# Optimization experiments

Hardware: AMD Instinct MI355X
Metric: run time of the kernel (lower is better)

Reference implementation:

```python
import jax, jax.numpy as jnp
import numpy as np

R = 4          # self.radius
NS = 256       # self.out_num_samples


def conv2d(x, w, b=None, padding=1, dilation=1):
    out = jax.lax.conv_general_dilated(
        x, w, window_strides=(1, 1),
        padding=[(padding, padding), (padding, padding)],
        rhs_dilation=(dilation, dilation),
        dimension_numbers=('NCHW', 'OIHW', 'NCHW'))
    if b is not None:
        out = out + b[None, :, None, None]
    return out


def depth_regression(logits):
    # softmax over 256 depth hypotheses, then expectation over a 9-wide
    # window centered at the argmax (clamped to [0, NS-1]).
    prob = jax.nn.softmax(logits, axis=1)                      # [B,256,H,W]
    amax = jnp.argmax(prob, axis=1, keepdims=True)             # [B,1,H,W] int
    offs = jnp.arange(-R, R + 1).reshape(1, 2 * R + 1, 1, 1)
    idx = jnp.clip(amax + offs, 0, NS - 1)                     # [B,9,H,W]
    p = jnp.take_along_axis(prob, idx, axis=1)                 # [B,9,H,W]
    num = jnp.sum(idx.astype(prob.dtype) * p, axis=1, keepdims=True)
    den = 1e-6 + jnp.sum(p, axis=1, keepdims=True)
    nd = (num / den) / (NS - 1.0)                              # [B,1,H,W]
    return nd, prob


def setup_inputs() -> dict:
    key = jax.random.key(0)
    ks = jax.random.split(key, 16)
    B, H, W = 4, 256, 320
    HD = 32            # hidden_dim
    CD = 32            # corr channels; input_dim = CD + 1 = 33
    CIN = HD + 1 + CD  # 65, GRU conv input channels

    def w(k, shape):
        fan = int(np.prod(shape[1:]))
        return (jax.random.normal(k, shape, jnp.float32) / np.sqrt(fan)).astype(jnp.float32)

    return {
        'hidden': jnp.tanh(jax.random.normal(ks[0], (B, HD, H, W), jnp.float32)),
        'normalized_depth': jax.random.uniform(ks[1], (B, 1, H, W), dtype=jnp.float32),
        'corr': jax.random.normal(ks[2], (B, CD, H, W), jnp.float32),
        # ConvGRU params (3x3, padding 1, with bias)
        'convz_w': w(ks[3], (HD, CIN, 3, 3)), 'convz_b': jnp.zeros((HD,), jnp.float32),
        'convr_w': w(ks[4], (HD, CIN, 3, 3)), 'convr_b': jnp.zeros((HD,), jnp.float32),
        'convq_w': w(ks[5], (HD, CIN, 3, 3)), 'convq_b': jnp.zeros((HD,), jnp.float32),
        # depth_head: 3x3 dil2 (no bias) -> 1x1 (no bias) -> 1x1 (bias)
        'dh1_w': w(ks[6], (32, HD, 3, 3)),
        'dh2_w': w(ks[7], (64, 32, 1, 1)),
        'dh3_w': w(ks[8], (NS, 64, 1, 1)), 'dh3_b': jnp.zeros((NS,), jnp.float32),
        # confidence_head: 3x3 dil2 (no bias) -> 1x1 (bias)
        'ch1_w': w(ks[9], (32, HD, 3, 3)),
        'ch2_w': w(ks[10], (1, 32, 1, 1)), 'ch2_b': jnp.zeros((1,), jnp.float32),
    }


def reference(hidden, normalized_depth, corr,
              convz_w, convz_b, convr_w, convr_b, convq_w, convq_b,
              dh1_w, dh2_w, dh3_w, dh3_b, ch1_w, ch2_w, ch2_b):
    # cat = [normalized_depth, corr]
    x = jnp.concatenate([normalized_depth, corr], axis=1)      # [B,33,H,W]
    # ConvGRU (confidence=None branch)
    hx = jnp.concatenate([hidden, x], axis=1)                  # [B,65,H,W]
    z = jax.nn.sigmoid(conv2d(hx, convz_w, convz_b))
    r = jax.nn.sigmoid(conv2d(hx, convr_w, convr_b))
    q = jnp.tanh(conv2d(jnp.concatenate([r * hidden, x], axis=1), convq_w, convq_b))
    h = (1.0 - z) * hidden + z * q                             # [B,32,H,W]
    # confidence head (confidence_flag=True)
    conf0 = conv2d(jax.nn.relu(conv2d(h, ch1_w, padding=2, dilation=2)),
                   ch2_w, ch2_b, padding=0)                    # [B,1,H,W]
    conf = jax.nn.sigmoid(conf0)
    # depth head
    t = jax.nn.relu(conv2d(h, dh1_w, padding=2, dilation=2))
    t = jax.nn.relu(conv2d(t, dh2_w, padding=0))
    logits = conv2d(t, dh3_w, dh3_b, padding=0)                # [B,256,H,W]
    nd, prob = depth_regression(logits)
    return h, nd, prob, conf, conf0
```

## Files before the change

### kernel.cpp

```cpp
#include <hip/hip_runtime.h>

#define WDT 320
#define HGT 256
#define HWSZ 81920
#define NPIX 327680

__device__ __forceinline__ float sigm(float x){ return 1.0f/(1.0f + __expf(-x)); }
__device__ __forceinline__ float tanh_(float x){
  float e = __expf(-2.0f*fabsf(x));
  float t = (1.0f - e)/(1.0f + e);
  return x < 0.0f ? -t : t;
}

__global__ __launch_bounds__(256) void k_wprep(
    const float* __restrict__ zw, const float* __restrict__ rw,
    const float* __restrict__ qw, const float* __restrict__ d1w,
    const float* __restrict__ c1w, const float* __restrict__ d2w,
    const float* __restrict__ d3w,
    float* __restrict__ W1, float* __restrict__ W2, float* __restrict__ W3,
    float* __restrict__ Wd2, float* __restrict__ Wd3)
{
  const int N1 = 9*65*64, N2 = 9*65*32, N3 = 9*32*64, N4 = 32*64, N5 = 64*256;
  int i = blockIdx.x*256 + threadIdx.x;
  if (i < N1){
    int cin = i / 576, r = i % 576;
    int tap = r >> 6, co = r & 63;
    float v = (co < 32) ? zw[(size_t)(co*65 + cin)*9 + tap]
                        : rw[(size_t)((co-32)*65 + cin)*9 + tap];
    W1[i] = v;
  } else if (i < N1 + N2){
    int j = i - N1;
    int cin = j / 288, r = j % 288;
    int tap = r >> 5, co = r & 31;
    W2[j] = qw[(size_t)(co*65 + cin)*9 + tap];
  } else if (i < N1 + N2 + N3){
    int j = i - (N1 + N2);
    int cin = j / 576, r = j % 576;
    int tap = r >> 6, co = r & 63;
    float v = (co < 32) ? d1w[(size_t)(co*32 + cin)*9 + tap]
                        : c1w[(size_t)((co-32)*32 + cin)*9 + tap];
    W3[j] = v;
  } else if (i < N1 + N2 + N3 + N4){
    int j = i - (N1 + N2 + N3);
    int cin = j >> 6, co = j & 63;
    Wd2[j] = d2w[co*32 + cin];
  } else if (i < N1 + N2 + N3 + N4 + N5){
    int j = i - (N1 + N2 + N3 + N4);
    int cin = j >> 8, co = j & 255;
    Wd3[j] = d3w[co*64 + cin];
  }
}


__global__ __launch_bounds__(256) void k_gru1(
    const float* __restrict__ hidden, const float* __restrict__ ndp,
    const float* __restrict__ corr, const float* __restrict__ W1,
    const float* __restrict__ zb, const float* __restrict__ rb,
    float* __restrict__ zpl, float* __restrict__ rhpl)
{
  int bid = blockIdx.x;
  int pb = (bid & 7)*160 + (bid >> 3);
  int p = pb*256 + threadIdx.x;
  int row = p / WDT;
  int x = p - row*WDT;
  int yimg = row & (HGT-1);
  int b = __builtin_amdgcn_readfirstlane(row >> 8);
  int q = p - b*HWSZ;
  int vo[9]; float mf[9];
  #pragma unroll
  for (int ty=0; ty<3; ++ty){
    #pragma unroll
    for (int tx=0; tx<3; ++tx){
      int dy = ty-1, dx = tx-1;
      bool ok = ((unsigned)(yimg+dy) < (unsigned)HGT) && ((unsigned)(x+dx) < (unsigned)WDT);
      vo[ty*3+tx] = ok ? (q + dy*WDT + dx) : q;
      mf[ty*3+tx] = ok ? 1.0f : 0.0f;
    }
  }
  const float* hb = hidden + (size_t)b*32*HWSZ;
  const float* cb = corr   + (size_t)b*32*HWSZ;
  const float* nb = ndp    + (size_t)b*HWSZ;
  float acc[64];
  #pragma unroll
  for (int i=0;i<64;++i) acc[i]=0.f;
  #pragma unroll 1
  for (int c=0;c<32;++c){
    const float* src = hb + (size_t)c*HWSZ;
    const float* wr  = W1 + c*576;
    #pragma unroll
    for (int t=0;t<9;++t){
      float vv = src[vo[t]] * mf[t];
      const float* w = wr + t*64;
      #pragma unroll
      for (int i=0;i<64;++i) acc[i] = fmaf(w[i], vv, acc[i]);
    }
  }
  {
    const float* wr = W1 + 32*576;
    #pragma unroll
    for (int t=0;t<9;++t){
      float vv = nb[vo[t]] * mf[t];
      const float* w = wr + t*64;
      #pragma unroll
      for (int i=0;i<64;++i) acc[i] = fmaf(w[i], vv, acc[i]);
    }
  }
  #pragma unroll 1
  for (int c=0;c<32;++c){
    const float* src = cb + (size_t)c*HWSZ;
    const float* wr  = W1 + (33+c)*576;
    #pragma unroll
    for (int t=0;t<9;++t){
      float vv = src[vo[t]] * mf[t];
      const float* w = wr + t*64;
      #pragma unroll
      for (int i=0;i<64;++i) acc[i] = fmaf(w[i], vv, acc[i]);
    }
  }
  #pragma unroll
  for (int c=0;c<32;++c)
    zpl[(size_t)c*NPIX + p] = sigm(acc[c] + zb[c]);
  #pragma unroll
  for (int c=0;c<32;++c){
    float r = sigm(acc[32+c] + rb[c]);
    rhpl[(size_t)c*NPIX + p] = r * hb[q + (size_t)c*HWSZ];
  }
}

__global__ __launch_bounds__(256) void k_gru2(
    const float* __restrict__ hidden, const float* __restrict__ ndp,
    const float* __restrict__ corr, const float* __restrict__ rhpl,
    const float* __restrict__ zpl, const float* __restrict__ W2,
    const float* __restrict__ qb, float* __restrict__ out_h)
{
  int bid = blockIdx.x;
  int pb = (bid & 7)*160 + (bid >> 3);
  int p = pb*256 + threadIdx.x;
  int row = p / WDT;
  int x = p - row*WDT;
  int yimg = row & (HGT-1);
  int b = __builtin_amdgcn_readfirstlane(row >> 8);
  int q = p - b*HWSZ;
  int vo[9]; float mf[9];
  #pragma unroll
  for (int ty=0; ty<3; ++ty){
    #pragma unroll
    for (int tx=0; tx<3; ++tx){
      int dy = ty-1, dx = tx-1;
      bool ok = ((unsigned)(yimg+dy) < (unsigned)HGT) && ((unsigned)(x+dx) < (unsigned)WDT);
      vo[ty*3+tx] = ok ? (q + dy*WDT + dx) : q;
      mf[ty*3+tx] = ok ? 1.0f : 0.0f;
    }
  }
  const float* hb = hidden + (size_t)b*32*HWSZ;
  const float* cb = corr   + (size_t)b*32*HWSZ;
  const float* nb = ndp    + (size_t)b*HWSZ;
  const float* rb_ = rhpl  + (size_t)b*HWSZ;
  float acc[32];
  #pragma unroll
  for (int i=0;i<32;++i) acc[i]=0.f;
  #pragma unroll 1
  for (int c=0;c<32;++c){
    const float* src = rb_ + (size_t)c*NPIX;
    const float* wr  = W2 + c*288;
    #pragma unroll
    for (int t=0;t<9;++t){
      float vv = src[vo[t]] * mf[t];
      const float* w = wr + t*32;
      #pragma unroll
      for (int i=0;i<32;++i) acc[i] = fmaf(w[i], vv, acc[i]);
    }
  }
  {
    const float* wr = W2 + 32*288;
    #pragma unroll
    for (int t=0;t<9;++t){
      float vv = nb[vo[t]] * mf[t];
      const float* w = wr + t*32;
      #pragma unroll
      for (int i=0;i<32;++i) acc[i] = fmaf(w[i], vv, acc[i]);
    }
  }
  #pragma unroll 1
  for (int c=0;c<32;++c){
    const float* src = cb + (size_t)c*HWSZ;
    const float* wr  = W2 + (33+c)*288;
    #pragma unroll
    for (int t=0;t<9;++t){
      float vv = src[vo[t]] * mf[t];
      const float* w = wr + t*32;
      #pragma unroll
      for (int i=0;i<32;++i) acc[i] = fmaf(w[i], vv, acc[i]);
    }
  }
  #pragma unroll
  for (int c=0;c<32;++c){
    float qv = tanh_(acc[c] + qb[c]);
    float z  = zpl[(size_t)c*NPIX + p];
    float h0 = hb[q + (size_t)c*HWSZ];
    out_h[(size_t)b*32*HWSZ + (size_t)c*HWSZ + q] = (1.0f - z)*h0 + z*qv;
  }
}

__global__ __launch_bounds__(256) void k_heads(
    const float* __restrict__ out_h, const float* __restrict__ W3,
    const float* __restrict__ c2w, const float* __restrict__ c2b,
    float* __restrict__ t1pl, float* __restrict__ out_conf, float* __restrict__ out_conf0)
{
  int bid = blockIdx.x;
  int pb = (bid & 7)*160 + (bid >> 3);
  int p = pb*256 + threadIdx.x;
  int row = p / WDT;
  int x = p - row*WDT;
  int yimg = row & (HGT-1);
  int b = __builtin_amdgcn_readfirstlane(row >> 8);
  int q = p - b*HWSZ;
  int vo[9]; float mf[9];
  #pragma unroll
  for (int ty=0; ty<3; ++ty){
    #pragma unroll
    for (int tx=0; tx<3; ++tx){
      int dy = (ty-1)*2, dx = (tx-1)*2;
      bool ok = ((unsigned)(yimg+dy) < (unsigned)HGT) && ((unsigned)(x+dx) < (unsigned)WDT);
      vo[ty*3+tx] = ok ? (q + dy*WDT + dx) : q;
      mf[ty*3+tx] = ok ? 1.0f : 0.0f;
    }
  }
  const float* hb = out_h + (size_t)b*32*HWSZ;
  float acc[64];
  #pragma unroll
  for (int i=0;i<64;++i) acc[i]=0.f;
  #pragma unroll 1
  for (int c=0;c<32;++c){
    const float* src = hb + (size_t)c*HWSZ;
    const float* wr  = W3 + c*576;
    #pragma unroll
    for (int t=0;t<9;++t){
      float vv = src[vo[t]] * mf[t];
      const float* w = wr + t*64;
      #pragma unroll
      for (int i=0;i<64;++i) acc[i] = fmaf(w[i], vv, acc[i]);
    }
  }
  #pragma unroll
  for (int c=0;c<32;++c)
    t1pl[(size_t)c*NPIX + p] = fmaxf(acc[c], 0.f);
  float conf0 = c2b[0];
  #pragma unroll
  for (int i=0;i<32;++i)
    conf0 = fmaf(fmaxf(acc[32+i], 0.f), c2w[i], conf0);
  out_conf0[p] = conf0;
  out_conf[p]  = sigm(conf0);
}

__global__ __launch_bounds__(256) void k_depth(
    const float* __restrict__ t1pl, const float* __restrict__ Wd2,
    const float* __restrict__ Wd3, const float* __restrict__ d3b,
    float* __restrict__ out_prob, float* __restrict__ out_nd)
{
  __shared__ float t2l[64][65];
  __shared__ float redA[4][64];
  __shared__ int   redI[4][64];
  __shared__ float redB[4][64];
  __shared__ float redC[4][64];
  int tid = threadIdx.x, lane = tid & 63;
  int wvu = __builtin_amdgcn_readfirstlane(tid >> 6);
  int p = blockIdx.x*64 + lane;
  float a1[16];
  #pragma unroll
  for (int i=0;i<16;++i) a1[i]=0.f;
  const float* Wd2b = Wd2 + wvu*16;
  #pragma unroll 2
  for (int c=0;c<32;++c){
    float v = t1pl[(size_t)c*NPIX + p];
    const float* w = Wd2b + c*64;
    #pragma unroll
    for (int i=0;i<16;++i) a1[i] = fmaf(w[i], v, a1[i]);
  }
  #pragma unroll
  for (int i=0;i<16;++i) t2l[lane][wvu*16+i] = fmaxf(a1[i], 0.f);
  __syncthreads();
  float acc[64];
  #pragma unroll
  for (int i=0;i<64;++i) acc[i]=0.f;
  const float* Wd3b = Wd3 + wvu*64;
  #pragma unroll 2
  for (int c=0;c<64;++c){
    float v = t2l[lane][c];
    const float* w = Wd3b + c*256;
    #pragma unroll
    for (int i=0;i<64;++i) acc[i] = fmaf(w[i], v, acc[i]);
  }
  const float* bb = d3b + wvu*64;
  float mx = -1e30f; int am = 0;
  #pragma unroll
  for (int i=0;i<64;++i){
    float l = acc[i] + bb[i];
    acc[i] = l;
    if (l > mx){ mx = l; am = wvu*64+i; }
  }
  redA[wvu][lane] = mx; redI[wvu][lane] = am;
  __syncthreads();
  float gmx = redA[0][lane]; int gam = redI[0][lane];
  #pragma unroll
  for (int w2=1; w2<4; ++w2){
    float m = redA[w2][lane]; int a = redI[w2][lane];
    if (m > gmx || (m == gmx && a < gam)){ gmx = m; gam = a; }
  }
  float s = 0.f;
  #pragma unroll
  for (int i=0;i<64;++i){
    float e = __expf(acc[i] - gmx);
    acc[i] = e; s += e;
  }
  redB[wvu][lane] = s;
  __syncthreads();
  float gs = redB[0][lane] + redB[1][lane] + redB[2][lane] + redB[3][lane];
  float inv = 1.0f / gs;
  int b = p / HWSZ;
  int qq = p - b*HWSZ;
  size_t obase = (size_t)b*256*HWSZ + qq;
  int lo = gam - 4, hi = gam + 4;
  float num = 0.f, den = 0.f;
  #pragma unroll
  for (int i=0;i<64;++i){
    int m = wvu*64 + i;
    float pr = acc[i] * inv;
    out_prob[obase + (size_t)m*HWSZ] = pr;
    int mlt = (m >= lo && m <= hi) ? 1 : 0;
    if (m == 0 && lo < 0) mlt = 1 - lo;
    if (m == 255 && hi > 255) mlt = hi - 254;
    num += (float)(m*mlt) * pr;
    den += (float)mlt * pr;
  }
  redA[wvu][lane] = num; redC[wvu][lane] = den;
  __syncthreads();
  if (wvu == 0){
    float tn = redA[0][lane]+redA[1][lane]+redA[2][lane]+redA[3][lane];
    float td = redC[0][lane]+redC[1][lane]+redC[2][lane]+redC[3][lane];
    out_nd[p] = (tn / (1e-6f + td)) * (1.0f/255.0f);
  }
}

extern "C" void kernel_launch(void* const* d_in, const int* in_sizes, int n_in,
                              void* d_out, int out_size, void* d_ws, size_t ws_size,
                              hipStream_t stream)
{
  const float* hidden = (const float*)d_in[0];
  const float* ndp    = (const float*)d_in[1];
  const float* corr   = (const float*)d_in[2];
  const float* zw  = (const float*)d_in[3];
  const float* zb  = (const float*)d_in[4];
  const float* rw  = (const float*)d_in[5];
  const float* rb  = (const float*)d_in[6];
  const float* qw  = (const float*)d_in[7];
  const float* qb  = (const float*)d_in[8];
  const float* d1w = (const float*)d_in[9];
  const float* d2w = (const float*)d_in[10];
  const float* d3w = (const float*)d_in[11];
  const float* d3b = (const float*)d_in[12];
  const float* c1w = (const float*)d_in[13];
  const float* c2w = (const float*)d_in[14];
  const float* c2b = (const float*)d_in[15];
  float* out = (float*)d_out;

  float* ws   = (float*)d_ws;
  float* zpl  = ws;
  float* rhpl = ws + 10485760;
  float* t1pl = ws + 20971520;
  float* W1   = ws + 31457280;
  float* W2   = W1 + 37440;
  float* W3   = W2 + 18720;
  float* Wd2  = W3 + 18432;
  float* Wd3  = Wd2 + 2048;

  float* out_h     = out;
  float* out_nd    = out + 10485760;
  float* out_prob  = out + 10813440;
  float* out_conf  = out + 94699520;
  float* out_conf0 = out + 95027200;

  k_wprep<<<364, 256, 0, stream>>>(zw, rw, qw, d1w, c1w, d2w, d3w, W1, W2, W3, Wd2, Wd3);
  k_gru1 <<<NPIX/256, 256, 0, stream>>>(hidden, ndp, corr, W1, zb, rb, zpl, rhpl);
  k_gru2 <<<NPIX/256, 256, 0, stream>>>(hidden, ndp, corr, rhpl, zpl, W2, qb, out_h);
  k_heads<<<NPIX/256, 256, 0, stream>>>(out_h, W3, c2w, c2b, t1pl, out_conf, out_conf0);
  k_depth<<<NPIX/64, 256, 0, stream>>>(t1pl, Wd2, Wd3, d3b, out_prob, out_nd);
}
```

Before: 1.261 ms.

## Stage GRU and head conv weights through double-buffered LDS

Restructures the three direct-conv kernels to copy weight chunks of 8 input channels into a double-buffered shared-memory tile, with a barrier per chunk, instead of reading weights straight from global memory. The channel loops are merged into one chunked loop, and the 9 tap values are loaded before the FMA block. This aims to cut global/cache traffic for weights, but it replaces uniform scalar weight loads with LDS reads and adds barriers and shared-memory pressure that can lower occupancy.

Result: slower. 1.363 ms (+8.1%).

```diff
diff --git a/kernel.cpp b/kernel.cpp
--- a/kernel.cpp
+++ b/kernel.cpp
@@ -58,6 +58,7 @@
     const float* __restrict__ zb, const float* __restrict__ rb,
     float* __restrict__ zpl, float* __restrict__ rhpl)
 {
+  __shared__ float wlds[2][8*576];
   int bid = blockIdx.x;
   int pb = (bid & 7)*160 + (bid >> 3);
   int p = pb*256 + threadIdx.x;
@@ -80,42 +81,44 @@
   const float* hb = hidden + (size_t)b*32*HWSZ;
   const float* cb = corr   + (size_t)b*32*HWSZ;
   const float* nb = ndp    + (size_t)b*HWSZ;
+
+  auto stage = [&](int k){
+    int nf = ((k==8)?1:8)*576;
+    const float* g = W1 + k*(8*576);
+    float* l = wlds[k&1];
+    for (int j = (int)threadIdx.x*4; j < nf; j += 1024)
+      *(float4*)&l[j] = *(const float4*)&g[j];
+  };
+
   float acc[64];
   #pragma unroll
   for (int i=0;i<64;++i) acc[i]=0.f;
+
+  stage(0);
+  __syncthreads();
   #pragma unroll 1
-  for (int c=0;c<32;++c){
-    const float* src = hb + (size_t)c*HWSZ;
-    const float* wr  = W1 + c*576;
-    #pragma unroll
-    for (int t=0;t<9;++t){
-      float vv = src[vo[t]] * mf[t];
-      const float* w = wr + t*64;
-      #pragma unroll
-      for (int i=0;i<64;++i) acc[i] = fmaf(w[i], vv, acc[i]);
-    }
-  }
-  {
-    const float* wr = W1 + 32*576;
-    #pragma unroll
-    for (int t=0;t<9;++t){
-      float vv = nb[vo[t]] * mf[t];
-      const float* w = wr + t*64;
-      #pragma unroll
-      for (int i=0;i<64;++i) acc[i] = fmaf(w[i], vv, acc[i]);
-    }
-  }
-  #pragma unroll 1
-  for (int c=0;c<32;++c){
-    const float* src = cb + (size_t)c*HWSZ;
-    const float* wr  = W1 + (33+c)*576;
-    #pragma unroll
-    for (int t=0;t<9;++t){
-      float vv = src[vo[t]] * mf[t];
-      const float* w = wr + t*64;
-      #pragma unroll
-      for (int i=0;i<64;++i) acc[i] = fmaf(w[i], vv, acc[i]);
-    }
+  for (int k=0;k<9;++k){
+    if (k < 8) stage(k+1);
+    const float* wlc = wlds[k&1];
+    int np = (k==8)?1:8;
+    #pragma unroll 1
+    for (int cl=0; cl<np; ++cl){
+      int c = k*8 + cl;
+      const float* src;
+      if (c < 32)       src = hb + (size_t)c*HWSZ;
+      else if (c == 32) src = nb;
+      else              src = cb + (size_t)(c-33)*HWSZ;
+      float v[9];
+      #pragma unroll
+      for (int t=0;t<9;++t) v[t] = src[vo[t]] * mf[t];
+      const float* wp = wlc + cl*576;
+      #pragma unroll
+      for (int t=0;t<9;++t){
+        #pragma unroll
+        for (int i=0;i<64;++i) acc[i] = fmaf(wp[t*64+i], v[t], acc[i]);
+      }
+    }
+    __syncthreads();
   }
   #pragma unroll
   for (int c=0;c<32;++c)
@@ -133,6 +136,7 @@
     const float* __restrict__ zpl, const float* __restrict__ W2,
     const float* __restrict__ qb, float* __restrict__ out_h)
 {
+  __shared__ float wlds[2][8*288];
   int bid = blockIdx.x;
   int pb = (bid & 7)*160 + (bid >> 3);
   int p = pb*256 + threadIdx.x;
@@ -152,46 +156,48 @@
       mf[ty*3+tx] = ok ? 1.0f : 0.0f;
     }
   }
-  const float* hb = hidden + (size_t)b*32*HWSZ;
-  const float* cb = corr   + (size_t)b*32*HWSZ;
-  const float* nb = ndp    + (size_t)b*HWSZ;
-  const float* rb_ = rhpl  + (size_t)b*HWSZ;
+  const float* hb  = hidden + (size_t)b*32*HWSZ;
+  const float* cb  = corr   + (size_t)b*32*HWSZ;
+  const float* nb  = ndp    + (size_t)b*HWSZ;
+  const float* rb_ = rhpl   + (size_t)b*HWSZ;
+
+  auto stage = [&](int k){
+    int nf = ((k==8)?1:8)*288;
+    const float* g = W2 + k*(8*288);
+    float* l = wlds[k&1];
+    for (int j = (int)threadIdx.x*4; j < nf; j += 1024)
+      *(float4*)&l[j] = *(const float4*)&g[j];
+  };
+
   float acc[32];
   #pragma unroll
   for (int i=0;i<32;++i) acc[i]=0.f;
+
+  stage(0);
+  __syncthreads();
   #pragma unroll 1
-  for (int c=0;c<32;++c){
-    const float* src = rb_ + (size_t)c*NPIX;
-    const float* wr  = W2 + c*288;
-    #pragma unroll
-    for (int t=0;t<9;++t){
-      float vv = src[vo[t]] * mf[t];
-      const float* w = wr + t*32;
-      #pragma unroll
-      for (int i=0;i<32;++i) acc[i] = fmaf(w[i], vv, acc[i]);
-    }
-  }
-  {
-    const float* wr = W2 + 32*288;
-    #pragma unroll
-    for (int t=0;t<9;++t){
-      float vv = nb[vo[t]] * mf[t];
-      const float* w = wr + t*32;
-      #pragma unroll
-      for (int i=0;i<32;++i) acc[i] = fmaf(w[i], vv, acc[i]);
-    }
-  }
-  #pragma unroll 1
-  for (int c=0;c<32;++c){
-    const float* src = cb + (size_t)c*HWSZ;
-    const float* wr  = W2 + (33+c)*288;
-    #pragma unroll
-    for (int t=0;t<9;++t){
-      float vv = src[vo[t]] * mf[t];
-      const float* w = wr + t*32;
-      #pragma unroll
-      for (int i=0;i<32;++i) acc[i] = fmaf(w[i], vv, acc[i]);
-    }
+  for (int k=0;k<9;++k){
+    if (k < 8) stage(k+1);
+    const float* wlc = wlds[k&1];
+    int np = (k==8)?1:8;
+    #pragma unroll 1
+    for (int cl=0; cl<np; ++cl){
+      int c = k*8 + cl;
+      const float* src;
+      if (c < 32)       src = rb_ + (size_t)c*NPIX;
+      else if (c == 32) src = nb;
+      else              src = cb + (size_t)(c-33)*HWSZ;
+      float v[9];
+      #pragma unroll
+      for (int t=0;t<9;++t) v[t] = src[vo[t]] * mf[t];
+      const float* wp = wlc + cl*288;
+      #pragma unroll
+      for (int t=0;t<9;++t){
+        #pragma unroll
+        for (int i=0;i<32;++i) acc[i] = fmaf(wp[t*32+i], v[t], acc[i]);
+      }
+    }
+    __syncthreads();
   }
   #pragma unroll
   for (int c=0;c<32;++c){
@@ -207,6 +213,7 @@
     const float* __restrict__ c2w, const float* __restrict__ c2b,
     float* __restrict__ t1pl, float* __restrict__ out_conf, float* __restrict__ out_conf0)
 {
+  __shared__ float wlds[2][8*576];
   int bid = blockIdx.x;
   int pb = (bid & 7)*160 + (bid >> 3);
   int p = pb*256 + threadIdx.x;
@@ -227,20 +234,39 @@
     }
   }
   const float* hb = out_h + (size_t)b*32*HWSZ;
+
+  auto stage = [&](int k){
+    const float* g = W3 + k*(8*576);
+    float* l = wlds[k&1];
+    for (int j = (int)threadIdx.x*4; j < 8*576; j += 1024)
+      *(float4*)&l[j] = *(const float4*)&g[j];
+  };
+
   float acc[64];
   #pragma unroll
   for (int i=0;i<64;++i) acc[i]=0.f;
+
+  stage(0);
+  __syncthreads();
   #pragma unroll 1
-  for (int c=0;c<32;++c){
-    const float* src = hb + (size_t)c*HWSZ;
-    const float* wr  = W3 + c*576;
-    #pragma unroll
-    for (int t=0;t<9;++t){
-      float vv = src[vo[t]] * mf[t];
-      const float* w = wr + t*64;
-      #pragma unroll
-      for (int i=0;i<64;++i) acc[i] = fmaf(w[i], vv, acc[i]);
-    }
+  for (int k=0;k<4;++k){
+    if (k < 3) stage(k+1);
+    const float* wlc = wlds[k&1];
+    #pragma unroll 1
+    for (int cl=0; cl<8; ++cl){
+      int c = k*8 + cl;
+      const float* src = hb + (size_t)c*HWSZ;
+      float v[9];
+      #pragma unroll
+      for (int t=0;t<9;++t) v[t] = src[vo[t]] * mf[t];
+      const float* wp = wlc + cl*576;
+      #pragma unroll
+      for (int t=0;t<9;++t){
+        #pragma unroll
+        for (int i=0;i<64;++i) acc[i] = fmaf(wp[t*64+i], v[t], acc[i]);
+      }
+    }
+    __syncthreads();
   }
   #pragma unroll
   for (int c=0;c<32;++c)
```
